# Kernel tuning notes

Measured on AMD Instinct MI355X. Metric: run time of the kernel, lower is better.

## Reference

```python
import jax, jax.numpy as jnp
import numpy as np

B, T, C = 2, 4096, 2048
HS = 64
DW, DA, DV, DG = 128, 128, 64, 224


def setup_inputs() -> dict:
    key = jax.random.key(0)
    ks = jax.random.split(key, 32)
    s = 0.02  # small weight scale to keep activations in a sane range
    inp = {
        'x': jax.random.normal(ks[0], (B, T, C), jnp.float32),
        'v_first': jax.random.normal(ks[1], (B, T, C), jnp.float32),
        'x_r': jax.random.uniform(ks[2], (C,), jnp.float32),
        'x_w': jax.random.uniform(ks[3], (C,), jnp.float32),
        'x_k': jax.random.uniform(ks[4], (C,), jnp.float32),
        'x_v': jax.random.uniform(ks[5], (C,), jnp.float32),
        'x_a': jax.random.uniform(ks[6], (C,), jnp.float32),
        'x_g': jax.random.uniform(ks[7], (C,), jnp.float32),
        'w0': jax.random.normal(ks[8], (C,), jnp.float32),
        'w1': jax.random.normal(ks[9], (C, DW), jnp.float32) * s,
        'w2': jax.random.normal(ks[10], (DW, C), jnp.float32) * s,
        'a0': jax.random.normal(ks[11], (C,), jnp.float32),
        'a1': jax.random.normal(ks[12], (C, DA), jnp.float32) * s,
        'a2': jax.random.normal(ks[13], (DA, C), jnp.float32) * s,
        'v0': jax.random.normal(ks[14], (C,), jnp.float32),
        'v1': jax.random.normal(ks[15], (C, DV), jnp.float32) * s,
        'v2': jax.random.normal(ks[16], (DV, C), jnp.float32) * s,
        'g1': jax.random.normal(ks[17], (C, DG), jnp.float32) * s,
        'g2': jax.random.normal(ks[18], (DG, C), jnp.float32) * s,
        'k_k': jax.random.normal(ks[19], (C,), jnp.float32) * 0.1 + 0.71,
        'k_a': jnp.full((C,), 1.02, jnp.float32),
        'Wr': jax.random.normal(ks[20], (C, C), jnp.float32) * s,
        'Wk': jax.random.normal(ks[21], (C, C), jnp.float32) * s,
        'Wv': jax.random.normal(ks[22], (C, C), jnp.float32) * s,
        'head_size': HS,
    }
    return inp


def reference(x, v_first, x_r, x_w, x_k, x_v, x_a, x_g,
              w0, w1, w2, a0, a1, a2, v0, v1, v2, g1, g2,
              k_k, k_a, Wr, Wk, Wv, head_size):
    Bd, Td, Cd = x.shape
    H = Cd // head_size
    # time shift: prepend zero frame, drop last
    xprev = jnp.concatenate([jnp.zeros_like(x[:, :1]), x[:, :-1]], axis=1)
    xx = xprev - x
    xr = x + xx * x_r
    xw = x + xx * x_w
    xk = x + xx * x_k
    xv = x + xx * x_v
    xa = x + xx * x_a
    xg = x + xx * x_g
    r = xr @ Wr.T                                   # [B,T,C]
    w = -jax.nn.softplus(-(w0 + jnp.tanh(xw @ w1) @ w2)) - 0.5
    k = xk @ Wk.T
    v = xv @ Wv.T
    # layer_id = 1 != 0  ->  mix with v_first
    v = v + (v_first - v) * jax.nn.sigmoid(v0 + (xv @ v1) @ v2)
    a = jax.nn.sigmoid(a0 + (xa @ a1) @ a2)
    g = jax.nn.sigmoid(xg @ g1) @ g2
    kk = k * k_k
    kk4 = kk.reshape(Bd, Td, H, head_size)
    nrm = jnp.linalg.norm(kk4, axis=-1, keepdims=True)
    kk = (kk4 / jnp.maximum(nrm, 1e-12)).reshape(Bd, Td, Cd)
    k = k * (1.0 + (a - 1.0) * k_a)
    return (r, w, k, v, a, g, kk, v_first)
```

## Files before the change

kernel.cpp:

```cpp
#include <hip/hip_runtime.h>
#include <hip/hip_bf16.h>

#define MTOT 8192
#define TLEN 4096
#define CDIM 2048
#define SLOT ((size_t)MTOT * CDIM)

typedef __attribute__((ext_vector_type(4))) float f32x4;
typedef __attribute__((ext_vector_type(8))) __bf16 bf16x8;

__device__ __forceinline__ short f2bf(float f) {
  __hip_bfloat16 h = __float2bfloat16(f);
  return __builtin_bit_cast(short, h);
}

__device__ __forceinline__ float sigm(float x) { return 1.f / (1.f + expf(-x)); }

__device__ __forceinline__ void gload16(const void* g, void* l) {
  __builtin_amdgcn_global_load_lds(
      (__attribute__((address_space(1))) void*)g,
      (__attribute__((address_space(3))) void*)l, 16, 0, 0);
}

__device__ __forceinline__ void gemm_core(
    const short* __restrict__ A, int lda,
    const short* __restrict__ Bt, int ldb,
    int K, int m0, int n0,
    short* As, short* Bs, f32x4 acc[4][4])
{
  const int tid  = threadIdx.x;
  const int lane = tid & 63;
  const int wv   = tid >> 6;
  const int wy   = wv >> 1;
  const int wx   = wv & 1;
  const int quad = lane >> 4;
  const int m16  = lane & 15;

  const f32x4 zero = {0.f, 0.f, 0.f, 0.f};
  #pragma unroll
  for (int i = 0; i < 4; ++i)
    #pragma unroll
    for (int j = 0; j < 4; ++j)
      acc[i][j] = zero;

  const int e0 = (wv * 64 + lane) * 8;
  const int e1 = e0 + 2048;
  const int r0 = e0 >> 5, c0 = e0 & 31;
  const int r1 = e1 >> 5, c1 = e1 & 31;
  const int lb0 = wv * 512;
  const int lb1 = 2048 + wv * 512;

  const short* pa0 = A  + (size_t)(m0 + r0) * lda + c0;
  const short* pa1 = A  + (size_t)(m0 + r1) * lda + c1;
  const short* pb0 = Bt + (size_t)(n0 + r0) * ldb + c0;
  const short* pb1 = Bt + (size_t)(n0 + r1) * ldb + c1;

  for (int k0 = 0; k0 < K; k0 += 32) {
    gload16(pa0 + k0, As + lb0);
    gload16(pa1 + k0, As + lb1);
    gload16(pb0 + k0, Bs + lb0);
    gload16(pb1 + k0, Bs + lb1);
    __syncthreads();

    bf16x8 af[4], bfr[4];
    #pragma unroll
    for (int mi = 0; mi < 4; ++mi)
      af[mi] = *(const bf16x8*)(As + (wy*64 + mi*16 + m16)*32 + quad*8);
    #pragma unroll
    for (int ni = 0; ni < 4; ++ni)
      bfr[ni] = *(const bf16x8*)(Bs + (wx*64 + ni*16 + m16)*32 + quad*8);

    #pragma unroll
    for (int mi = 0; mi < 4; ++mi)
      #pragma unroll
      for (int ni = 0; ni < 4; ++ni)
        acc[mi][ni] = __builtin_amdgcn_mfma_f32_16x16x32_bf16(
            af[mi], bfr[ni], acc[mi][ni], 0, 0, 0);
    __syncthreads();
  }
}

__global__ __launch_bounds__(256) void mix_kernel(
    const float* __restrict__ x, const float* __restrict__ vfin,
    const float* __restrict__ cr, const float* __restrict__ cw,
    const float* __restrict__ ck, const float* __restrict__ cv,
    const float* __restrict__ ca, const float* __restrict__ cg,
    short* __restrict__ xr, short* __restrict__ xw, short* __restrict__ xk,
    short* __restrict__ xv, short* __restrict__ xa, short* __restrict__ xg,
    float* __restrict__ vfout)
{
  const size_t i = (size_t)blockIdx.x * 256 + threadIdx.x;
  const size_t e = i * 4;
  const int c = (int)(e & (CDIM - 1));
  const size_t m = e >> 11;
  const int t = (int)(m & (TLEN - 1));
  const float4 xc = *(const float4*)(x + e);
  float4 xp = make_float4(0.f, 0.f, 0.f, 0.f);
  if (t > 0) xp = *(const float4*)(x + e - CDIM);
  const float d0 = xp.x - xc.x, d1 = xp.y - xc.y;
  const float d2 = xp.z - xc.z, d3 = xp.w - xc.w;

  *(float4*)(vfout + e) = *(const float4*)(vfin + e);

  #define EMIT(coef, dst) { \
    const float4 cf = *(const float4*)((coef) + c); \
    short4 s; \
    s.x = f2bf(xc.x + d0 * cf.x); \
    s.y = f2bf(xc.y + d1 * cf.y); \
    s.z = f2bf(xc.z + d2 * cf.z); \
    s.w = f2bf(xc.w + d3 * cf.w); \
    *(short4*)((dst) + e) = s; }
  EMIT(cr, xr) EMIT(cw, xw) EMIT(ck, xk) EMIT(cv, xv) EMIT(ca, xa) EMIT(cg, xg)
  #undef EMIT
}

__global__ __launch_bounds__(256) void cvt_big(
    const float* __restrict__ Wr, const float* __restrict__ Wk,
    const float* __restrict__ Wv,
    short* __restrict__ br, short* __restrict__ bk, short* __restrict__ bv)
{
  const int z = blockIdx.y;
  const float* src = (z == 0) ? Wr : (z == 1) ? Wk : Wv;
  short* dst = (z == 0) ? br : (z == 1) ? bk : bv;
  const size_t e = ((size_t)blockIdx.x * 256 + threadIdx.x) * 4;
  const float4 v = *(const float4*)(src + e);
  short4 s;
  s.x = f2bf(v.x); s.y = f2bf(v.y); s.z = f2bf(v.z); s.w = f2bf(v.w);
  *(short4*)(dst + e) = s;
}

__global__ __launch_bounds__(256) void wtrans(
    const float* __restrict__ w1, const float* __restrict__ a1,
    const float* __restrict__ v1, const float* __restrict__ g1,
    const float* __restrict__ w2, const float* __restrict__ a2,
    const float* __restrict__ v2, const float* __restrict__ g2,
    short* __restrict__ w1t, short* __restrict__ a1t,
    short* __restrict__ v1t, short* __restrict__ g1t,
    short* __restrict__ w2t, short* __restrict__ a2t,
    short* __restrict__ v2t, short* __restrict__ g2t)
{
  const int task = blockIdx.y;
  const int i = blockIdx.x * 256 + threadIdx.x;
  switch (task) {
    case 0: if (i < 128*2048) { int d=i>>11, c=i&2047; w1t[i]=f2bf(w1[(size_t)c*128+d]); } break;
    case 1: if (i < 128*2048) { int d=i>>11, c=i&2047; a1t[i]=f2bf(a1[(size_t)c*128+d]); } break;
    case 2: if (i < 128*2048) { int d=i>>11, c=i&2047; v1t[i]=(d<64)?f2bf(v1[(size_t)c*64+d]):(short)0; } break;
    case 3: if (i < 256*2048) { int d=i>>11, c=i&2047; g1t[i]=(d<224)?f2bf(g1[(size_t)c*224+d]):(short)0; } break;
    case 4: if (i < 2048*128) { int c=i>>7, d=i&127; w2t[i]=f2bf(w2[(size_t)d*2048+c]); } break;
    case 5: if (i < 2048*128) { int c=i>>7, d=i&127; a2t[i]=f2bf(a2[(size_t)d*2048+c]); } break;
    case 6: if (i < 2048*64)  { int c=i>>6, d=i&63;  v2t[i]=f2bf(v2[(size_t)d*2048+c]); } break;
    case 7: if (i < 2048*224) { int c=i/224, d=i-c*224; g2t[i]=f2bf(g2[(size_t)d*2048+c]); } break;
  }
}

__global__ __launch_bounds__(256) void gemm_big(
    const short* __restrict__ xr, const short* __restrict__ xk,
    const short* __restrict__ xv,
    const short* __restrict__ Wr, const short* __restrict__ Wk,
    const short* __restrict__ Wv,
    float* __restrict__ out)
{
  __shared__ short As[4096], Bs[4096];
  const int z = blockIdx.z;
  const short* A  = (z == 0) ? xr : (z == 1) ? xk : xv;
  const short* Bt = (z == 0) ? Wr : (z == 1) ? Wk : Wv;
  float* O = (z == 0) ? out : (z == 1) ? out + 2*SLOT : out + 3*SLOT;
  const int m0 = blockIdx.x * 128, n0 = blockIdx.y * 128;
  f32x4 acc[4][4];
  gemm_core(A, CDIM, Bt, CDIM, CDIM, m0, n0, As, Bs, acc);

  const int tid=threadIdx.x, lane=tid&63, wv=tid>>6;
  const int wy=wv>>1, wx=wv&1, quad=lane>>4, m16=lane&15;
  #pragma unroll
  for (int mi = 0; mi < 4; ++mi) {
    const int mb = m0 + wy*64 + mi*16 + quad*4;
    #pragma unroll
    for (int ni = 0; ni < 4; ++ni) {
      const int n = n0 + wx*64 + ni*16 + m16;
      #pragma unroll
      for (int r = 0; r < 4; ++r)
        O[(size_t)(mb + r) * CDIM + n] = acc[mi][ni][r];
    }
  }
}

__global__ __launch_bounds__(256) void gemm_s1(
    const short* __restrict__ xw, const short* __restrict__ xa,
    const short* __restrict__ xv, const short* __restrict__ xg,
    const short* __restrict__ w1t, const short* __restrict__ a1t,
    const short* __restrict__ v1t, const short* __restrict__ g1t,
    short* __restrict__ hw, short* __restrict__ ha,
    short* __restrict__ hv, short* __restrict__ hg)
{
  const int z = blockIdx.z;
  const int nb = blockIdx.y;
  if (z != 3 && nb != 0) return;
  __shared__ short As[4096], Bs[4096];
  const short* A  = (z==0) ? xw  : (z==1) ? xa  : (z==2) ? xv  : xg;
  const short* Bt = (z==0) ? w1t : (z==1) ? a1t : (z==2) ? v1t : g1t;
  short* H        = (z==0) ? hw  : (z==1) ? ha  : (z==2) ? hv  : hg;
  const int Nreal = (z==2) ? 64 : (z==3) ? 224 : 128;
  const int m0 = blockIdx.x * 128, n0 = nb * 128;
  f32x4 acc[4][4];
  gemm_core(A, CDIM, Bt, CDIM, CDIM, m0, n0, As, Bs, acc);

  const int tid=threadIdx.x, lane=tid&63, wv=tid>>6;
  const int wy=wv>>1, wx=wv&1, quad=lane>>4, m16=lane&15;
  #pragma unroll
  for (int mi = 0; mi < 4; ++mi) {
    const int mb = m0 + wy*64 + mi*16 + quad*4;
    #pragma unroll
    for (int ni = 0; ni < 4; ++ni) {
      const int n = n0 + wx*64 + ni*16 + m16;
      if (n < Nreal) {
        #pragma unroll
        for (int r = 0; r < 4; ++r) {
          float v = acc[mi][ni][r];
          if (z == 0) v = tanhf(v);
          else if (z == 3) v = sigm(v);
          H[(size_t)(mb + r) * Nreal + n] = f2bf(v);
        }
      }
    }
  }
}

__global__ __launch_bounds__(256) void gemm_s2(
    const short* __restrict__ hw, const short* __restrict__ ha,
    const short* __restrict__ hv, const short* __restrict__ hg,
    const short* __restrict__ w2t, const short* __restrict__ a2t,
    const short* __restrict__ v2t, const short* __restrict__ g2t,
    const float* __restrict__ w0, const float* __restrict__ a0,
    const float* __restrict__ v0, const float* __restrict__ vfirst,
    float* __restrict__ out)
{
  __shared__ short As[4096], Bs[4096];
  const int z = blockIdx.z;
  const short* A  = (z==0) ? hw  : (z==1) ? ha  : (z==2) ? hv  : hg;
  const short* Bt = (z==0) ? w2t : (z==1) ? a2t : (z==2) ? v2t : g2t;
  const int K = (z==2) ? 64 : (z==3) ? 224 : 128;
  const int m0 = blockIdx.x * 128, n0 = blockIdx.y * 128;
  f32x4 acc[4][4];
  gemm_core(A, K, Bt, K, K, m0, n0, As, Bs, acc);

  const int tid=threadIdx.x, lane=tid&63, wv=tid>>6;
  const int wy=wv>>1, wx=wv&1, quad=lane>>4, m16=lane&15;
  #pragma unroll
  for (int mi = 0; mi < 4; ++mi) {
    const int mb = m0 + wy*64 + mi*16 + quad*4;
    #pragma unroll
    for (int ni = 0; ni < 4; ++ni) {
      const int n = n0 + wx*64 + ni*16 + m16;
      #pragma unroll
      for (int r = 0; r < 4; ++r) {
        const float val = acc[mi][ni][r];
        const size_t idx = (size_t)(mb + r) * CDIM + n;
        if (z == 0) {
          float zz = w0[n] + val;
          float sp = fmaxf(-zz, 0.f) + log1pf(expf(-fabsf(zz)));
          out[SLOT + idx] = -sp - 0.5f;
        } else if (z == 1) {
          out[4*SLOT + idx] = sigm(a0[n] + val);
        } else if (z == 2) {
          const float gate = sigm(v0[n] + val);
          const float vr = out[3*SLOT + idx];
          out[3*SLOT + idx] = vr + (vfirst[idx] - vr) * gate;
        } else {
          out[5*SLOT + idx] = val;
        }
      }
    }
  }
}

__global__ __launch_bounds__(256) void fin_k(
    const float* __restrict__ kkc, const float* __restrict__ kac,
    float* __restrict__ out)
{
  const int wid  = blockIdx.x * 4 + (threadIdx.x >> 6);
  const int lane = threadIdx.x & 63;
  const size_t m = (size_t)(wid >> 5);
  const int h = wid & 31;
  const int c = h * 64 + lane;
  const size_t idx = m * CDIM + c;
  const float kraw = out[2*SLOT + idx];
  const float a    = out[4*SLOT + idx];
  const float kkv  = kraw * kkc[c];
  float ss = kkv * kkv;
  #pragma unroll
  for (int o = 32; o >= 1; o >>= 1) ss += __shfl_xor(ss, o, 64);
  const float nrm = sqrtf(ss);
  out[6*SLOT + idx] = kkv / fmaxf(nrm, 1e-12f);
  out[2*SLOT + idx] = kraw * (1.f + (a - 1.f) * kac[c]);
}

extern "C" void kernel_launch(void* const* d_in, const int* in_sizes, int n_in,
                              void* d_out, int out_size, void* d_ws, size_t ws_size,
                              hipStream_t stream) {
  (void)in_sizes; (void)n_in; (void)out_size; (void)ws_size;
  const float* x   = (const float*)d_in[0];
  const float* vf  = (const float*)d_in[1];
  const float* x_r = (const float*)d_in[2];
  const float* x_w = (const float*)d_in[3];
  const float* x_k = (const float*)d_in[4];
  const float* x_v = (const float*)d_in[5];
  const float* x_a = (const float*)d_in[6];
  const float* x_g = (const float*)d_in[7];
  const float* w0  = (const float*)d_in[8];
  const float* w1  = (const float*)d_in[9];
  const float* w2  = (const float*)d_in[10];
  const float* a0  = (const float*)d_in[11];
  const float* a1  = (const float*)d_in[12];
  const float* a2  = (const float*)d_in[13];
  const float* v0  = (const float*)d_in[14];
  const float* v1  = (const float*)d_in[15];
  const float* v2  = (const float*)d_in[16];
  const float* g1  = (const float*)d_in[17];
  const float* g2  = (const float*)d_in[18];
  const float* k_k = (const float*)d_in[19];
  const float* k_a = (const float*)d_in[20];
  const float* Wr  = (const float*)d_in[21];
  const float* Wk  = (const float*)d_in[22];
  const float* Wv  = (const float*)d_in[23];

  float* out = (float*)d_out;

  short* xr_b = (short*)(out + 1*SLOT);
  short* xw_b = xr_b + SLOT;
  short* xk_b = (short*)(out + 4*SLOT);
  short* xv_b = xk_b + SLOT;
  short* xa_b = (short*)(out + 5*SLOT);
  short* xg_b = xa_b + SLOT;

  char* wsp = (char*)d_ws;
  size_t off = 0;
  #define ALLOC(var, bytes) short* var = (short*)(wsp + off); off += (((size_t)(bytes)) + 255) & ~(size_t)255;
  ALLOC(Wr_b, (size_t)CDIM*CDIM*2)
  ALLOC(Wk_b, (size_t)CDIM*CDIM*2)
  ALLOC(Wv_b, (size_t)CDIM*CDIM*2)
  ALLOC(w1t, 128*2048*2)
  ALLOC(a1t, 128*2048*2)
  ALLOC(v1t, 128*2048*2)
  ALLOC(g1t, 256*2048*2)
  ALLOC(w2t, 2048*128*2)
  ALLOC(a2t, 2048*128*2)
  ALLOC(v2t, 2048*64*2)
  ALLOC(g2t, 2048*224*2)
  ALLOC(hw, (size_t)MTOT*128*2)
  ALLOC(ha, (size_t)MTOT*128*2)
  ALLOC(hv, (size_t)MTOT*64*2)
  ALLOC(hg, (size_t)MTOT*224*2)
  #undef ALLOC

  mix_kernel<<<dim3(16384), 256, 0, stream>>>(
      x, vf, x_r, x_w, x_k, x_v, x_a, x_g,
      xr_b, xw_b, xk_b, xv_b, xa_b, xg_b, out + 7*SLOT);

  cvt_big<<<dim3(4096, 3), 256, 0, stream>>>(Wr, Wk, Wv, Wr_b, Wk_b, Wv_b);

  wtrans<<<dim3(2048, 8), 256, 0, stream>>>(
      w1, a1, v1, g1, w2, a2, v2, g2,
      w1t, a1t, v1t, g1t, w2t, a2t, v2t, g2t);

  gemm_big<<<dim3(64, 16, 3), 256, 0, stream>>>(
      xr_b, xk_b, xv_b, Wr_b, Wk_b, Wv_b, out);

  gemm_s1<<<dim3(64, 2, 4), 256, 0, stream>>>(
      xw_b, xa_b, xv_b, xg_b, w1t, a1t, v1t, g1t, hw, ha, hv, hg);

  gemm_s2<<<dim3(64, 16, 4), 256, 0, stream>>>(
      hw, ha, hv, hg, w2t, a2t, v2t, g2t, w0, a0, v0, vf, out);

  fin_k<<<dim3(65536), 256, 0, stream>>>(k_k, k_a, out);
}
```

Baseline: 1.410 ms.

## Replace big projection GEMM with 256x256-tile double-buffered LDS-pipelined kernel

Replaces the 128x128-tile r/k/v projection GEMM with a 512-thread kernel that computes 256x256 output tiles. It double-buffers K-slices in 128KB of LDS through direct global-to-LDS loads with XOR swizzling. Loads for the next slice are interleaved with MFMA phases using explicit barriers, waitcnts and setprio. The aim is more data reuse per loaded tile and overlap of memory traffic with matrix math. The cost is heavy LDS use, which limits occupancy to one block per CU, and fragile hand-scheduled synchronisation.

```diff
diff --git a/kernel.cpp b/kernel.cpp
--- a/kernel.cpp
+++ b/kernel.cpp
@@ -153,33 +153,156 @@
   }
 }
 
-__global__ __launch_bounds__(256) void gemm_big(
+__global__ __launch_bounds__(512, 2) void gemm_big2(
     const short* __restrict__ xr, const short* __restrict__ xk,
     const short* __restrict__ xv,
     const short* __restrict__ Wr, const short* __restrict__ Wk,
     const short* __restrict__ Wv,
     float* __restrict__ out)
 {
-  __shared__ short As[4096], Bs[4096];
+  __shared__ short As[32768];
+  __shared__ short Bs[32768];
+
   const int z = blockIdx.z;
   const short* A  = (z == 0) ? xr : (z == 1) ? xk : xv;
   const short* Bt = (z == 0) ? Wr : (z == 1) ? Wk : Wv;
   float* O = (z == 0) ? out : (z == 1) ? out + 2*SLOT : out + 3*SLOT;
-  const int m0 = blockIdx.x * 128, n0 = blockIdx.y * 128;
-  f32x4 acc[4][4];
-  gemm_core(A, CDIM, Bt, CDIM, CDIM, m0, n0, As, Bs, acc);
-
-  const int tid=threadIdx.x, lane=tid&63, wv=tid>>6;
-  const int wy=wv>>1, wx=wv&1, quad=lane>>4, m16=lane&15;
-  #pragma unroll
-  for (int mi = 0; mi < 4; ++mi) {
-    const int mb = m0 + wy*64 + mi*16 + quad*4;
+
+  const int m0 = blockIdx.x * 256, n0 = blockIdx.y * 256;
+  const int tid  = threadIdx.x;
+  const int lane = tid & 63, wid = tid >> 6;
+  const int wm = wid >> 2, wn = wid & 3;
+  const int quad = lane >> 4, m16 = lane & 15;
+
+  const int srow = tid >> 2;
+  const int csrc = (((tid & 3) ^ ((tid >> 3) & 3)) << 3);
+  const size_t aoff = (size_t)(m0 + srow) * CDIM + csrc;
+  const size_t boff = (size_t)(n0 + srow) * CDIM + csrc;
+  const int lbase = wid * 512;
+
+  const int fslot = ((quad ^ ((m16 >> 1) & 3)) << 3);
+  const int abase = (wm*128 + m16) * 32 + fslot;
+  const int bbase = (wn*64  + m16) * 32 + fslot;
+
+  f32x4 acc[8][4];
+  const f32x4 zf = {0.f, 0.f, 0.f, 0.f};
+  #pragma unroll
+  for (int i = 0; i < 8; ++i)
+    #pragma unroll
+    for (int j = 0; j < 4; ++j) acc[i][j] = zf;
+
+  #define STG(REG, BASEP, OFF, KOFF) do { \
+    gload16((BASEP) + (OFF) + (KOFF), (REG) + lbase); \
+    gload16((BASEP) + (OFF) + (KOFF) + (size_t)128*CDIM, (REG) + lbase + 4096); \
+  } while (0)
+
+  STG(As + 0,    A,  aoff, 0);
+  STG(Bs + 0,    Bt, boff, 0);
+  STG(As + 8192, A,  aoff, 32);
+  STG(Bs + 8192, Bt, boff, 32);
+  asm volatile("s_waitcnt vmcnt(4)" ::: "memory");
+  __builtin_amdgcn_s_barrier();
+  __builtin_amdgcn_sched_barrier(0);
+
+  const int NT = CDIM / 64;
+  for (int t = 0; t < NT; ++t) {
+    const int db = (t & 1) << 14;
+    const int nb = 16384 - db;
+    const int kn = t*64 + 64;
+    const bool pf = (kn < CDIM);
+    short* Ar0 = As + db;
+    short* Br0 = Bs + db;
+    short* Ar1 = As + db + 8192;
+    short* Br1 = Bs + db + 8192;
+
+    bf16x8 af[8], b0, b1;
+
+    #pragma unroll
+    for (int mi = 0; mi < 8; ++mi)
+      af[mi] = *(const bf16x8*)(Ar0 + abase + mi*512);
+    b0 = *(const bf16x8*)(Br0 + bbase + 0*512);
+    b1 = *(const bf16x8*)(Br0 + bbase + 1*512);
+    if (pf) STG(As + nb, A, aoff, kn);
+    __builtin_amdgcn_s_barrier();
+    asm volatile("s_waitcnt lgkmcnt(0)" ::: "memory");
+    __builtin_amdgcn_sched_barrier(0);
+    __builtin_amdgcn_s_setprio(1);
+    #pragma unroll
+    for (int mi = 0; mi < 8; ++mi)
+      acc[mi][0] = __builtin_amdgcn_mfma_f32_16x16x32_bf16(af[mi], b0, acc[mi][0], 0, 0, 0);
+    #pragma unroll
+    for (int mi = 0; mi < 8; ++mi)
+      acc[mi][1] = __builtin_amdgcn_mfma_f32_16x16x32_bf16(af[mi], b1, acc[mi][1], 0, 0, 0);
+    __builtin_amdgcn_s_setprio(0);
+    __builtin_amdgcn_s_barrier();
+
+    b0 = *(const bf16x8*)(Br0 + bbase + 2*512);
+    b1 = *(const bf16x8*)(Br0 + bbase + 3*512);
+    if (pf) STG(Bs + nb, Bt, boff, kn);
+    __builtin_amdgcn_s_barrier();
+    asm volatile("s_waitcnt lgkmcnt(0)" ::: "memory");
+    __builtin_amdgcn_sched_barrier(0);
+    __builtin_amdgcn_s_setprio(1);
+    #pragma unroll
+    for (int mi = 0; mi < 8; ++mi)
+      acc[mi][2] = __builtin_amdgcn_mfma_f32_16x16x32_bf16(af[mi], b0, acc[mi][2], 0, 0, 0);
+    #pragma unroll
+    for (int mi = 0; mi < 8; ++mi)
+      acc[mi][3] = __builtin_amdgcn_mfma_f32_16x16x32_bf16(af[mi], b1, acc[mi][3], 0, 0, 0);
+    __builtin_amdgcn_s_setprio(0);
+    if (pf) asm volatile("s_waitcnt vmcnt(4)" ::: "memory");
+    else    asm volatile("s_waitcnt vmcnt(0)" ::: "memory");
+    __builtin_amdgcn_s_barrier();
+    __builtin_amdgcn_sched_barrier(0);
+
+    #pragma unroll
+    for (int mi = 0; mi < 8; ++mi)
+      af[mi] = *(const bf16x8*)(Ar1 + abase + mi*512);
+    b0 = *(const bf16x8*)(Br1 + bbase + 0*512);
+    b1 = *(const bf16x8*)(Br1 + bbase + 1*512);
+    if (pf) STG(As + nb + 8192, A, aoff, kn + 32);
+    __builtin_amdgcn_s_barrier();
+    asm volatile("s_waitcnt lgkmcnt(0)" ::: "memory");
+    __builtin_amdgcn_sched_barrier(0);
+    __builtin_amdgcn_s_setprio(1);
+    #pragma unroll
+    for (int mi = 0; mi < 8; ++mi)
+      acc[mi][0] = __builtin_amdgcn_mfma_f32_16x16x32_bf16(af[mi], b0, acc[mi][0], 0, 0, 0);
+    #pragma unroll
+    for (int mi = 0; mi < 8; ++mi)
+      acc[mi][1] = __builtin_amdgcn_mfma_f32_16x16x32_bf16(af[mi], b1, acc[mi][1], 0, 0, 0);
+    __builtin_amdgcn_s_setprio(0);
+    __builtin_amdgcn_s_barrier();
+
+    b0 = *(const bf16x8*)(Br1 + bbase + 2*512);
+    b1 = *(const bf16x8*)(Br1 + bbase + 3*512);
+    if (pf) STG(Bs + nb + 8192, Bt, boff, kn + 32);
+    __builtin_amdgcn_s_barrier();
+    asm volatile("s_waitcnt lgkmcnt(0)" ::: "memory");
+    __builtin_amdgcn_sched_barrier(0);
+    __builtin_amdgcn_s_setprio(1);
+    #pragma unroll
+    for (int mi = 0; mi < 8; ++mi)
+      acc[mi][2] = __builtin_amdgcn_mfma_f32_16x16x32_bf16(af[mi], b0, acc[mi][2], 0, 0, 0);
+    #pragma unroll
+    for (int mi = 0; mi < 8; ++mi)
+      acc[mi][3] = __builtin_amdgcn_mfma_f32_16x16x32_bf16(af[mi], b1, acc[mi][3], 0, 0, 0);
+    __builtin_amdgcn_s_setprio(0);
+    asm volatile("s_waitcnt vmcnt(4)" ::: "memory");
+    __builtin_amdgcn_s_barrier();
+    __builtin_amdgcn_sched_barrier(0);
+  }
+  #undef STG
+
+  #pragma unroll
+  for (int mi = 0; mi < 8; ++mi) {
+    const int row = m0 + wm*128 + mi*16 + quad*4;
     #pragma unroll
     for (int ni = 0; ni < 4; ++ni) {
-      const int n = n0 + wx*64 + ni*16 + m16;
+      const int col = n0 + wn*64 + ni*16 + m16;
       #pragma unroll
       for (int r = 0; r < 4; ++r)
-        O[(size_t)(mb + r) * CDIM + n] = acc[mi][ni][r];
+        O[(size_t)(row + r) * CDIM + col] = acc[mi][ni][r];
     }
   }
 }
@@ -362,7 +485,7 @@
       w1, a1, v1, g1, w2, a2, v2, g2,
       w1t, a1t, v1t, g1t, w2t, a2t, v2t, g2t);
 
-  gemm_big<<<dim3(64, 16, 3), 256, 0, stream>>>(
+  gemm_big2<<<dim3(32, 8, 3), 512, 0, stream>>>(
       xr_b, xk_b, xv_b, Wr_b, Wk_b, Wv_b, out);
 
   gemm_s1<<<dim3(64, 2, 4), 256, 0, stream>>>(
```

Measured after the change: 1.276 ms. 1.1x faster.
